# Optimization experiments

Measured on AMD Instinct MI355X. Metric: run time of the kernel, lower is better.

Reference implementation:

```python
import jax, jax.numpy as jnp
import numpy as np

EMB_DIM, D_H, BSZ, SEQ = 2048, 128, 4, 4096
HALF = D_H // 2


def apply_rope(x, sin, cos):
    # x: [b, s, d]; sin/cos: [s, d//2]; interleaved-pair rotation
    b, s, d = x.shape
    xr = x.reshape(b, s, d // 2, 2)
    x0, x1 = xr[..., 0], xr[..., 1]
    r0 = x0 * cos - x1 * sin
    r1 = x1 * cos + x0 * sin
    return jnp.stack([r0, r1], axis=-1).reshape(b, s, d)


def setup_inputs() -> dict:
    key = jax.random.key(0)
    kx, kq, kk, kv = jax.random.split(key, 4)
    x = jax.random.normal(kx, (BSZ, SEQ, EMB_DIM), dtype=jnp.float32)
    # causal mask (1 = attend, 0 = masked), matching mask[q,:] slicing in source
    mask = jnp.tril(jnp.ones((SEQ, SEQ), dtype=jnp.int32))
    # standard RoPE angle tables: [seq, d_h//2]
    inv_freq = 1.0 / (10000.0 ** (jnp.arange(HALF, dtype=jnp.float32) / HALF))
    angles = jnp.arange(SEQ, dtype=jnp.float32)[:, None] * inv_freq[None, :]
    sin, cos = jnp.sin(angles), jnp.cos(angles)
    scale = 1.0 / np.sqrt(EMB_DIM)
    W_Q = jax.random.normal(kq, (EMB_DIM, D_H), dtype=jnp.float32) * scale
    W_K = jax.random.normal(kk, (EMB_DIM, D_H), dtype=jnp.float32) * scale
    W_V = jax.random.normal(kv, (EMB_DIM, D_H), dtype=jnp.float32) * scale
    return {"x": x, "mask": mask, "sin": sin, "cos": cos,
            "W_Q": W_Q, "W_K": W_K, "W_V": W_V}


def reference(x, mask, sin, cos, W_Q, W_V, W_K):
    # QKV projections
    Q = apply_rope(x @ W_Q, sin, cos)  # [b, s, d_h]
    K = apply_rope(x @ W_K, sin, cos)  # [b, s, d_h]
    V = x @ W_V                        # [b, s, d_h]
    # The source's chunked loop is exactly full masked attention over all K/V.
    scores = jnp.einsum('bqd,bkd->bqk', Q, K) / jnp.sqrt(jnp.float32(D_H))
    scores = jnp.where(mask[None, :, :] == 0, -jnp.inf, scores)
    attn = jax.nn.softmax(scores, axis=-1)
    return jnp.einsum('bqk,bkd->bqd', attn, V)
```

## Files before the change

kernel.cpp:

```cpp
#include <hip/hip_runtime.h>
#include <stdint.h>
#include <stddef.h>

typedef __bf16 bf16;
typedef __bf16 bf16x8 __attribute__((ext_vector_type(8)));
typedef float f32x4 __attribute__((ext_vector_type(4)));
typedef unsigned int uint32x2 __attribute__((ext_vector_type(2)));
typedef unsigned int uint32x4 __attribute__((ext_vector_type(4)));

typedef const __attribute__((address_space(1))) uint32_t GU32;
typedef __attribute__((address_space(3))) uint32_t LU32;

__device__ __forceinline__ f32x4 mfma16(bf16x8 a, bf16x8 b, f32x4 c) {
  return __builtin_amdgcn_mfma_f32_16x16x32_bf16(a, b, c, 0, 0, 0);
}
__device__ __forceinline__ void gload16(const void* g, void* l) {
  __builtin_amdgcn_global_load_lds((GU32*)g, (LU32*)l, 16, 0, 0);
}

__global__ __launch_bounds__(256) void k_prep(const float* __restrict__ Wq,
                                              const float* __restrict__ Wk,
                                              const float* __restrict__ Wv,
                                              bf16* __restrict__ Wct) {
  __shared__ float tile[64][65];
  const int tid = threadIdx.x;
  const int widx = blockIdx.x >> 6, rem = blockIdx.x & 63;
  const int k0 = (rem >> 1) * 64, n0 = (rem & 1) * 64;
  const float* W = (widx == 0) ? Wq : (widx == 1) ? Wk : Wv;
  const int rg = tid >> 4, cq = tid & 15;
#pragma unroll
  for (int i = 0; i < 4; ++i) {
    int krow = i * 16 + rg;
    f32x4 v = *(const f32x4*)(W + (size_t)(k0 + krow) * 128 + n0 + cq * 4);
#pragma unroll
    for (int j = 0; j < 4; ++j) tile[krow][cq * 4 + j] = v[j];
  }
  __syncthreads();
#pragma unroll
  for (int i = 0; i < 4; ++i) {
    int nrow = i * 16 + rg;
    union { bf16 h[4]; uint32x2 u; } pk;
#pragma unroll
    for (int j = 0; j < 4; ++j) pk.h[j] = (bf16)tile[cq * 4 + j][nrow];
    *(uint32x2*)(Wct + (size_t)(widx * 128 + n0 + nrow) * 2048 + k0 + cq * 4) = pk.u;
  }
}

__global__ __launch_bounds__(256, 2) void k_proj(
    const float* __restrict__ x, const float* __restrict__ sint, const float* __restrict__ cost,
    const bf16* __restrict__ Wct, bf16* __restrict__ Qg, bf16* __restrict__ Kg,
    bf16* __restrict__ Vtg) {
  __shared__ __align__(16) uint8_t smem[65536];
  const int tid = threadIdx.x;
  const int lane = tid & 63, w = tid >> 6;
  const int l15 = lane & 15, l16 = lane >> 4;
  const int logical = (blockIdx.x & 7) * 64 + (blockIdx.x >> 3);
  const int nb = logical & 1, mb = logical >> 1;
  const int wm = w >> 1, wn = w & 1;
  const int arow = tid >> 2, aj = tid & 3;

  f32x4 acc[2][6] = {};
  f32x4 areg[4];

  const float* abase = x + (size_t)(mb * 64 + arow) * 2048 + aj * 16;

  auto stageB = [&](int buf, int ks) {
    uint8_t* bbm = smem + buf * 32768 + 8192;
    int k0 = ks * 64;
#pragma unroll
    for (int i = 0; i < 6; ++i) {
      int L = i * 4096 + tid * 16;
      int n = L >> 7, cp = (L >> 4) & 7;
      int cc = cp ^ (n & 7);
      const uint8_t* src = (const uint8_t*)Wct + (((size_t)(nb * 192 + n) * 2048 + k0 + cc * 8) << 1);
      gload16(src, bbm + i * 4096 + w * 1024);
    }
  };
  auto loadA = [&](int ks) {
    const f32x4* p = (const f32x4*)(abase + ks * 64);
#pragma unroll
    for (int i = 0; i < 4; ++i) areg[i] = p[i];
  };
  auto writeA = [&](int buf) {
    uint8_t* ab = smem + buf * 32768;
#pragma unroll
    for (int h = 0; h < 2; ++h) {
      union { bf16 v[8]; uint32x4 u; } pk;
#pragma unroll
      for (int e = 0; e < 8; ++e) pk.v[e] = (bf16)areg[h * 2 + (e >> 2)][e & 3];
      int c = aj * 2 + h;
      *(uint32x4*)(ab + arow * 128 + (((c ^ (arow & 7)) & 7) << 4)) = pk.u;
    }
  };
  auto compute = [&](int buf) {
    uint8_t* ab = smem + buf * 32768;
    uint8_t* bbm = ab + 8192;
#pragma unroll
    for (int kk = 0; kk < 2; ++kk) {
      bf16x8 af[2], bv[6];
#pragma unroll
      for (int mt = 0; mt < 2; ++mt) {
        int ml = wm * 32 + mt * 16 + l15;
        af[mt] = *(const bf16x8*)(ab + ml * 128 + (((kk * 4 + l16) ^ (ml & 7)) << 4));
      }
#pragma unroll
      for (int nt = 0; nt < 6; ++nt) {
        int nl = wn * 96 + nt * 16 + l15;
        bv[nt] = *(const bf16x8*)(bbm + nl * 128 + (((kk * 4 + l16) ^ (nl & 7)) << 4));
      }
#pragma unroll
      for (int mt = 0; mt < 2; ++mt)
#pragma unroll
        for (int nt = 0; nt < 6; ++nt)
          acc[mt][nt] = mfma16(af[mt], bv[nt], acc[mt][nt]);
    }
  };

  stageB(0, 0);
  loadA(0);
  writeA(0);
  __syncthreads();
  for (int ks = 0; ks < 32; ++ks) {
    int cur = ks & 1;
    if (ks + 1 < 32) { stageB(cur ^ 1, ks + 1); loadA(ks + 1); }
    compute(cur);
    if (ks + 1 < 32) writeA(cur ^ 1);
    __syncthreads();
  }

#pragma unroll
  for (int mt = 0; mt < 2; ++mt) {
    int gm = mb * 64 + wm * 32 + mt * 16 + l16 * 4;
    int bb = gm >> 12, s0 = gm & 4095;
#pragma unroll
    for (int nt = 0; nt < 6; ++nt) {
      int jcol = nb * 192 + wn * 96 + nt * 16 + l15;
      f32x4 v = acc[mt][nt];
      if (jcol < 256) {
        int p = (jcol & 127) >> 1;
        bool even = ((jcol & 1) == 0);
#pragma unroll
        for (int r = 0; r < 4; ++r) {
          float pv = __shfl_xor(v[r], 1);
          int s = s0 + r;
          float cs = cost[s * 64 + p], sn = sint[s * 64 + p];
          float nv = even ? (v[r] * cs - pv * sn) : (v[r] * cs + pv * sn);
          bf16 hb = (bf16)nv;
          if (jcol < 128) Qg[((size_t)(bb << 12) + s) * 128 + jcol] = hb;
          else            Kg[((size_t)(bb << 12) + s) * 128 + jcol - 128] = hb;
        }
      } else {
        int d = jcol - 256;
        union { bf16 h[4]; uint32x2 u; } pk;
#pragma unroll
        for (int r = 0; r < 4; ++r) pk.h[r] = (bf16)v[r];
        *(uint32x2*)((uint8_t*)Vtg + (((size_t)(bb << 7) + d) * 4096 + s0) * 2) = pk.u;
      }
    }
  }
}

__global__ __launch_bounds__(256, 2) void k_attn(
    const bf16* __restrict__ Qg, const bf16* __restrict__ Kg, const bf16* __restrict__ Vtg,
    float* __restrict__ PO, float* __restrict__ ML) {
  __shared__ __align__(16) uint8_t smem[81920];
  const int tid = threadIdx.x;
  const int lane = tid & 63, w = tid >> 6;
  const int l15 = lane & 15, l16 = lane >> 4;

  int gid = blockIdx.x;
  int b = gid / 80, rr = gid % 80;
  int j, c;
  if (rr < 8)       { j = rr;                 c = 0; }
  else if (rr < 24) { j = 8 + ((rr - 8) >> 1);  c = (rr - 8) & 1; }
  else if (rr < 48) { j = 16 + (rr - 24) / 3;   c = (rr - 24) % 3; }
  else              { j = 24 + ((rr - 48) >> 2); c = (rr - 48) & 3; }

  const int q0w = j * 128 + w * 32;
  const int kv_lo = c * 1024;
  const int kv_hi = min((c + 1) * 1024, (j + 1) * 128);
  const int T = (kv_hi - kv_lo) >> 6;

  bf16x8 qf[2][4];
#pragma unroll
  for (int qt = 0; qt < 2; ++qt)
#pragma unroll
    for (int kk = 0; kk < 4; ++kk)
      qf[qt][kk] = *(const bf16x8*)(Qg + ((size_t)(b << 12) + q0w + qt * 16 + l15) * 128 + kk * 32 + l16 * 8);

  f32x4 o[2][8] = {};
  float m_r[2] = {-1e30f, -1e30f};
  float l_r[2] = {0.f, 0.f};
  uint8_t* pb = smem + 65536 + w * 4096;

  auto stage = [&](int t) {
    uint8_t* kb = smem + (t & 1) * 32768;
    uint8_t* vb = kb + 16384;
    int kv0 = kv_lo + t * 64;
#pragma unroll
    for (int i = 0; i < 4; ++i) {
      int L = i * 4096 + tid * 16;
      {
        int kv = L >> 8, cp = (L >> 4) & 15, cc = cp ^ (kv & 7);
        const uint8_t* src = (const uint8_t*)Kg + ((size_t)((b << 12) + kv0 + kv) << 8) + (cc << 4);
        gload16(src, kb + i * 4096 + w * 1024);
      }
      {
        int d = L >> 7, cp = (L >> 4) & 7, cc = cp ^ (d & 7);
        const uint8_t* src = (const uint8_t*)Vtg + ((size_t)(((b << 7) + d) << 12) + kv0 + (cc << 3)) * 2;
        gload16(src, vb + i * 4096 + w * 1024);
      }
    }
  };

  stage(0);
  __syncthreads();

  for (int t = 0; t < T; ++t) {
    if (t + 1 < T) stage(t + 1);
    const int kv0 = kv_lo + t * 64;
    if (kv0 <= q0w + 31) {
      uint8_t* kb = smem + (t & 1) * 32768;
      uint8_t* vb = kb + 16384;
      f32x4 sfr[4][2] = {};
#pragma unroll
      for (int kk = 0; kk < 4; ++kk) {
#pragma unroll
        for (int kvt = 0; kvt < 4; ++kvt) {
          int kvl = kvt * 16 + l15;
          bf16x8 kf = *(const bf16x8*)(kb + (kvl << 8) + (((kk * 4 + l16) ^ (kvl & 7)) << 4));
#pragma unroll
          for (int qt = 0; qt < 2; ++qt)
            sfr[kvt][qt] = mfma16(kf, qf[qt][kk], sfr[kvt][qt]);
        }
      }
      const bool need_mask = (kv0 + 63 > q0w);
      const float scale = 0.08838834764831845f;
#pragma unroll
      for (int qt = 0; qt < 2; ++qt) {
        const int q = q0w + qt * 16 + l15;
        float pvv[4][4];
        float tmax = -1e30f;
#pragma unroll
        for (int kvt = 0; kvt < 4; ++kvt)
#pragma unroll
          for (int r = 0; r < 4; ++r) {
            float sv = sfr[kvt][qt][r] * scale;
            if (need_mask) {
              int kv = kv0 + kvt * 16 + l16 * 4 + r;
              if (kv > q) sv = -1e30f;
            }
            pvv[kvt][r] = sv;
            tmax = fmaxf(tmax, sv);
          }
        tmax = fmaxf(tmax, __shfl_xor(tmax, 16));
        tmax = fmaxf(tmax, __shfl_xor(tmax, 32));
        float mnew = fmaxf(m_r[qt], tmax);
        float corr = __expf(m_r[qt] - mnew);
        m_r[qt] = mnew;
        float rs = 0.f;
#pragma unroll
        for (int kvt = 0; kvt < 4; ++kvt)
#pragma unroll
          for (int r = 0; r < 4; ++r) {
            float p = __expf(pvv[kvt][r] - mnew);
            pvv[kvt][r] = p;
            rs += p;
          }
        rs += __shfl_xor(rs, 16);
        rs += __shfl_xor(rs, 32);
        l_r[qt] = l_r[qt] * corr + rs;
        const int qrow = qt * 16 + l15;
#pragma unroll
        for (int kvt = 0; kvt < 4; ++kvt) {
          union { bf16 h[4]; uint32x2 u; } pk;
#pragma unroll
          for (int r = 0; r < 4; ++r) pk.h[r] = (bf16)pvv[kvt][r];
          int kv2 = kvt * 32 + l16 * 8;
          *(uint32x2*)(pb + qrow * 128 + ((((kv2 >> 4) ^ (qrow & 7)) << 4) | (kv2 & 15))) = pk.u;
        }
#pragma unroll
        for (int r = 0; r < 4; ++r) {
          float cr = __shfl(corr, l16 * 4 + r);
#pragma unroll
          for (int dt = 0; dt < 8; ++dt) o[qt][dt][r] *= cr;
        }
      }
#pragma unroll
      for (int kvb = 0; kvb < 2; ++kvb) {
        bf16x8 pa[2];
#pragma unroll
        for (int qt = 0; qt < 2; ++qt) {
          int qrow = qt * 16 + l15;
          int kv2 = kvb * 64 + l16 * 16;
          pa[qt] = *(const bf16x8*)(pb + qrow * 128 + (((kv2 >> 4) ^ (qrow & 7)) << 4));
        }
#pragma unroll
        for (int dt = 0; dt < 8; ++dt) {
          int d = dt * 16 + l15;
          bf16x8 vf = *(const bf16x8*)(vb + (d << 7) + (((kvb * 4 + l16) ^ (d & 7)) << 4));
#pragma unroll
          for (int qt = 0; qt < 2; ++qt)
            o[qt][dt] = mfma16(pa[qt], vf, o[qt][dt]);
        }
      }
    }
    __syncthreads();
  }

  float* POb = PO + (size_t)((b * 32 + j) * 4 + c) * 16384;
#pragma unroll
  for (int qt = 0; qt < 2; ++qt)
#pragma unroll
    for (int dt = 0; dt < 8; ++dt)
#pragma unroll
      for (int r = 0; r < 4; ++r)
        POb[(w * 32 + qt * 16 + l16 * 4 + r) * 128 + dt * 16 + l15] = o[qt][dt][r];
  float* MLb = ML + (size_t)((b * 32 + j) * 4 + c) * 256;
  if (l16 == 0) {
#pragma unroll
    for (int qt = 0; qt < 2; ++qt) {
      MLb[w * 32 + qt * 16 + l15] = m_r[qt];
      MLb[128 + w * 32 + qt * 16 + l15] = l_r[qt];
    }
  }
}

__global__ void k_combine(const float* __restrict__ PO, const float* __restrict__ ML,
                          float* __restrict__ out) {
  int blk = blockIdx.x;
  int b = blk >> 5, j = blk & 31;
  int nc = 1 + (j >> 3);
  int t = threadIdx.x;
  int q = t >> 1, half = t & 1;
  const float* MLb = ML + (size_t)(b * 32 + j) * 4 * 256;
  float mv[4], lv[4];
  float ms = -1e30f;
  for (int cc = 0; cc < nc; ++cc) {
    mv[cc] = MLb[cc * 256 + q];
    lv[cc] = MLb[cc * 256 + 128 + q];
    ms = fmaxf(ms, mv[cc]);
  }
  float wgt[4];
  float den = 0.f;
  for (int cc = 0; cc < nc; ++cc) { wgt[cc] = __expf(mv[cc] - ms); den += wgt[cc] * lv[cc]; }
  float inv = 1.f / den;
  const float* POb = PO + (size_t)(b * 32 + j) * 4 * 16384 + q * 128 + half * 64;
  float* ob = out + ((size_t)(b << 12) + j * 128 + q) * 128 + half * 64;
  for (int d = 0; d < 64; d += 4) {
    f32x4 a = {0.f, 0.f, 0.f, 0.f};
    for (int cc = 0; cc < nc; ++cc) {
      f32x4 v = *(const f32x4*)(POb + cc * 16384 + d);
      a += v * wgt[cc];
    }
    a *= inv;
    *(f32x4*)(ob + d) = a;
  }
}

extern "C" void kernel_launch(void* const* d_in, const int* in_sizes, int n_in,
                              void* d_out, int out_size, void* d_ws, size_t ws_size,
                              hipStream_t stream) {
  const float* x = (const float*)d_in[0];
  const float* sint = (const float*)d_in[2];
  const float* cost = (const float*)d_in[3];
  const float* Wq = (const float*)d_in[4];
  const float* Wk = (const float*)d_in[5];
  const float* Wv = (const float*)d_in[6];
  uint8_t* ws = (uint8_t*)d_ws;

  bf16* Wct = (bf16*)(ws + 0x0);
  bf16* Qg  = (bf16*)(ws + 0x180000);
  bf16* Kg  = (bf16*)(ws + 0x580000);
  bf16* Vtg = (bf16*)(ws + 0x980000);
  float* PO = (float*)(ws + 0xD80000);
  float* ML = (float*)(ws + 0x2D80000);
  float* out = (float*)d_out;

  hipLaunchKernelGGL(k_prep, dim3(192), dim3(256), 0, stream, Wq, Wk, Wv, Wct);
  hipLaunchKernelGGL(k_proj, dim3(512), dim3(256), 0, stream, x, sint, cost, Wct, Qg, Kg, Vtg);
  hipLaunchKernelGGL(k_attn, dim3(320), dim3(256), 0, stream, Qg, Kg, Vtg, PO, ML);
  hipLaunchKernelGGL(k_combine, dim3(128), dim3(256), 0, stream, PO, ML, out);
}
```

Baseline: 140.7 us.

## Deepen projection GEMM pipeline with double register A buffers and manual waitcnts

Rewrites the k_proj main loop to prefetch x tiles two steps ahead into alternating register buffers. The loop is unrolled by two, and the full __syncthreads is replaced with explicit vmcnt/lgkmcnt waits plus s_barrier, so the newest A loads stay in flight across the barrier. The compute step now loads all LDS fragments for both k-substeps before issuing the MFMAs, and raises wave priority with s_setprio around the MFMA block. The aim is to hide global load latency in the projection GEMM, at the cost of more registers and reliance on hand-counted vmcnt values matching the compiler's load order.

```diff
diff --git a/kernel.cpp b/kernel.cpp
--- a/kernel.cpp
+++ b/kernel.cpp
@@ -60,7 +60,7 @@
   const int arow = tid >> 2, aj = tid & 3;
 
   f32x4 acc[2][6] = {};
-  f32x4 areg[4];
+  f32x4 regA[4], regB[4];
 
   const float* abase = x + (size_t)(mb * 64 + arow) * 2048 + aj * 16;
 
@@ -76,18 +76,18 @@
       gload16(src, bbm + i * 4096 + w * 1024);
     }
   };
-  auto loadA = [&](int ks) {
+  auto loadA = [&](int ks, f32x4* r) {
     const f32x4* p = (const f32x4*)(abase + ks * 64);
 #pragma unroll
-    for (int i = 0; i < 4; ++i) areg[i] = p[i];
+    for (int i = 0; i < 4; ++i) r[i] = p[i];
   };
-  auto writeA = [&](int buf) {
+  auto writeA = [&](int buf, const f32x4* r) {
     uint8_t* ab = smem + buf * 32768;
 #pragma unroll
     for (int h = 0; h < 2; ++h) {
       union { bf16 v[8]; uint32x4 u; } pk;
 #pragma unroll
-      for (int e = 0; e < 8; ++e) pk.v[e] = (bf16)areg[h * 2 + (e >> 2)][e & 3];
+      for (int e = 0; e < 8; ++e) pk.v[e] = (bf16)r[h * 2 + (e >> 2)][e & 3];
       int c = aj * 2 + h;
       *(uint32x4*)(ab + arow * 128 + (((c ^ (arow & 7)) & 7) << 4)) = pk.u;
     }
@@ -95,38 +95,68 @@
   auto compute = [&](int buf) {
     uint8_t* ab = smem + buf * 32768;
     uint8_t* bbm = ab + 8192;
+    bf16x8 af[2][2], bv[2][6];
 #pragma unroll
     for (int kk = 0; kk < 2; ++kk) {
-      bf16x8 af[2], bv[6];
 #pragma unroll
       for (int mt = 0; mt < 2; ++mt) {
         int ml = wm * 32 + mt * 16 + l15;
-        af[mt] = *(const bf16x8*)(ab + ml * 128 + (((kk * 4 + l16) ^ (ml & 7)) << 4));
+        af[kk][mt] = *(const bf16x8*)(ab + ml * 128 + (((kk * 4 + l16) ^ (ml & 7)) << 4));
       }
 #pragma unroll
       for (int nt = 0; nt < 6; ++nt) {
         int nl = wn * 96 + nt * 16 + l15;
-        bv[nt] = *(const bf16x8*)(bbm + nl * 128 + (((kk * 4 + l16) ^ (nl & 7)) << 4));
-      }
+        bv[kk][nt] = *(const bf16x8*)(bbm + nl * 128 + (((kk * 4 + l16) ^ (nl & 7)) << 4));
+      }
+    }
+    __builtin_amdgcn_s_setprio(1);
+#pragma unroll
+    for (int kk = 0; kk < 2; ++kk)
 #pragma unroll
       for (int mt = 0; mt < 2; ++mt)
 #pragma unroll
         for (int nt = 0; nt < 6; ++nt)
-          acc[mt][nt] = mfma16(af[mt], bv[nt], acc[mt][nt]);
-    }
+          acc[mt][nt] = mfma16(af[kk][mt], bv[kk][nt], acc[mt][nt]);
+    __builtin_amdgcn_s_setprio(0);
   };
 
+  loadA(0, regA);
   stageB(0, 0);
-  loadA(0);
-  writeA(0);
-  __syncthreads();
-  for (int ks = 0; ks < 32; ++ks) {
-    int cur = ks & 1;
-    if (ks + 1 < 32) { stageB(cur ^ 1, ks + 1); loadA(ks + 1); }
-    compute(cur);
-    if (ks + 1 < 32) writeA(cur ^ 1);
-    __syncthreads();
-  }
+  loadA(1, regB);
+  writeA(0, regA);
+  asm volatile("s_waitcnt vmcnt(4)" ::: "memory");
+  asm volatile("s_waitcnt lgkmcnt(0)" ::: "memory");
+  __builtin_amdgcn_s_barrier();
+
+  for (int ks = 0; ks < 30; ks += 2) {
+    {
+      stageB(1, ks + 1);
+      loadA(ks + 2, regA);
+      compute(0);
+      writeA(1, regB);
+      asm volatile("s_waitcnt vmcnt(4)" ::: "memory");
+      asm volatile("s_waitcnt lgkmcnt(0)" ::: "memory");
+      __builtin_amdgcn_s_barrier();
+    }
+    {
+      stageB(0, ks + 2);
+      loadA(ks + 3, regB);
+      compute(1);
+      writeA(0, regA);
+      asm volatile("s_waitcnt vmcnt(4)" ::: "memory");
+      asm volatile("s_waitcnt lgkmcnt(0)" ::: "memory");
+      __builtin_amdgcn_s_barrier();
+    }
+  }
+  {
+    stageB(1, 31);
+    compute(0);
+    writeA(1, regB);
+    asm volatile("s_waitcnt vmcnt(0)" ::: "memory");
+    asm volatile("s_waitcnt lgkmcnt(0)" ::: "memory");
+    __builtin_amdgcn_s_barrier();
+  }
+  compute(1);
 
 #pragma unroll
   for (int mt = 0; mt < 2; ++mt) {
```

Result: faster. 132.2 us (-6.0%).

## Pre-swizzle weights into MFMA fragment order and enlarge projection tiles to 128 rows

Applied to the files above, without the earlier changes.

The prep kernel now writes the bf16 weights directly in per-k-step MFMA fragment order, so the projection kernel can stage B with contiguous global-to-LDS loads and read fragments without XOR swizzling. The projection kernel moves to 512-thread blocks covering 128 rows with an 8-wave 2x4 layout, and raises wave priority around the MFMA section. The aims are to cut address arithmetic, get more A reuse per B tile and lower the block count, in exchange for more LDS per block (80 KB) and a launch bound that restricts registers.

```diff
diff --git a/kernel.cpp b/kernel.cpp
--- a/kernel.cpp
+++ b/kernel.cpp
@@ -21,7 +21,7 @@
 __global__ __launch_bounds__(256) void k_prep(const float* __restrict__ Wq,
                                               const float* __restrict__ Wk,
                                               const float* __restrict__ Wv,
-                                              bf16* __restrict__ Wct) {
+                                              bf16* __restrict__ WB) {
   __shared__ float tile[64][65];
   const int tid = threadIdx.x;
   const int widx = blockIdx.x >> 6, rem = blockIdx.x & 63;
@@ -37,82 +37,85 @@
   }
   __syncthreads();
 #pragma unroll
-  for (int i = 0; i < 4; ++i) {
-    int nrow = i * 16 + rg;
-    union { bf16 h[4]; uint32x2 u; } pk;
-#pragma unroll
-    for (int j = 0; j < 4; ++j) pk.h[j] = (bf16)tile[cq * 4 + j][nrow];
-    *(uint32x2*)(Wct + (size_t)(widx * 128 + n0 + nrow) * 2048 + k0 + cq * 4) = pk.u;
-  }
-}
-
-__global__ __launch_bounds__(256, 2) void k_proj(
+  for (int gi = 0; gi < 2; ++gi) {
+    int G = tid * 2 + gi;
+    int n_local = G >> 3, kg = G & 7;
+    union { bf16 h[8]; uint32x4 u; } pk;
+#pragma unroll
+    for (int j = 0; j < 8; ++j) pk.h[j] = (bf16)tile[kg * 8 + j][n_local];
+    int n_glob = widx * 128 + n0 + n_local;
+    int k_glob = k0 + kg * 8;
+    int nb = n_glob / 192, nr = n_glob % 192;
+    int ngl = nr >> 4, l15g = nr & 15;
+    int ks = k_glob >> 6, kk = (k_glob >> 5) & 1, l16g = (k_glob >> 3) & 3;
+    size_t gaddr = ((size_t)(nb * 32 + ks) * 1536) + ((ngl * 2 + kk) * 64 + l16g * 16 + l15g);
+    *(uint32x4*)((uint8_t*)WB + gaddr * 16) = pk.u;
+  }
+}
+
+__global__ __launch_bounds__(512, 4) void k_proj(
     const float* __restrict__ x, const float* __restrict__ sint, const float* __restrict__ cost,
-    const bf16* __restrict__ Wct, bf16* __restrict__ Qg, bf16* __restrict__ Kg,
+    const bf16* __restrict__ WB, bf16* __restrict__ Qg, bf16* __restrict__ Kg,
     bf16* __restrict__ Vtg) {
-  __shared__ __align__(16) uint8_t smem[65536];
+  __shared__ __align__(16) uint8_t smem[81920];
   const int tid = threadIdx.x;
   const int lane = tid & 63, w = tid >> 6;
   const int l15 = lane & 15, l16 = lane >> 4;
-  const int logical = (blockIdx.x & 7) * 64 + (blockIdx.x >> 3);
+  const int logical = (blockIdx.x & 7) * 32 + (blockIdx.x >> 3);
   const int nb = logical & 1, mb = logical >> 1;
-  const int wm = w >> 1, wn = w & 1;
+  const int wm = w >> 2, wn = w & 3;
   const int arow = tid >> 2, aj = tid & 3;
 
-  f32x4 acc[2][6] = {};
-  f32x4 areg[4];
-
-  const float* abase = x + (size_t)(mb * 64 + arow) * 2048 + aj * 16;
+  f32x4 acc[4][3] = {};
+  f32x4 ar[4];
+
+  const float* abase = x + (size_t)(mb * 128 + arow) * 2048 + aj * 16;
+  const uint8_t* wbase = (const uint8_t*)WB + (size_t)nb * 32 * 24576;
 
   auto stageB = [&](int buf, int ks) {
-    uint8_t* bbm = smem + buf * 32768 + 8192;
-    int k0 = ks * 64;
-#pragma unroll
-    for (int i = 0; i < 6; ++i) {
-      int L = i * 4096 + tid * 16;
-      int n = L >> 7, cp = (L >> 4) & 7;
-      int cc = cp ^ (n & 7);
-      const uint8_t* src = (const uint8_t*)Wct + (((size_t)(nb * 192 + n) * 2048 + k0 + cc * 8) << 1);
-      gload16(src, bbm + i * 4096 + w * 1024);
-    }
+    uint8_t* bbm = smem + 32768 + buf * 24576;
+    const uint8_t* src = wbase + (size_t)ks * 24576 + tid * 16;
+#pragma unroll
+    for (int i = 0; i < 3; ++i)
+      gload16(src + i * 8192, bbm + i * 8192 + tid * 16);
   };
   auto loadA = [&](int ks) {
     const f32x4* p = (const f32x4*)(abase + ks * 64);
 #pragma unroll
-    for (int i = 0; i < 4; ++i) areg[i] = p[i];
+    for (int i = 0; i < 4; ++i) ar[i] = p[i];
   };
   auto writeA = [&](int buf) {
-    uint8_t* ab = smem + buf * 32768;
+    uint8_t* ab = smem + buf * 16384;
 #pragma unroll
     for (int h = 0; h < 2; ++h) {
       union { bf16 v[8]; uint32x4 u; } pk;
 #pragma unroll
-      for (int e = 0; e < 8; ++e) pk.v[e] = (bf16)areg[h * 2 + (e >> 2)][e & 3];
+      for (int e = 0; e < 8; ++e) pk.v[e] = (bf16)ar[h * 2 + (e >> 2)][e & 3];
       int c = aj * 2 + h;
       *(uint32x4*)(ab + arow * 128 + (((c ^ (arow & 7)) & 7) << 4)) = pk.u;
     }
   };
   auto compute = [&](int buf) {
-    uint8_t* ab = smem + buf * 32768;
-    uint8_t* bbm = ab + 8192;
+    uint8_t* ab = smem + buf * 16384;
+    uint8_t* bbm = smem + 32768 + buf * 24576;
 #pragma unroll
     for (int kk = 0; kk < 2; ++kk) {
-      bf16x8 af[2], bv[6];
-#pragma unroll
-      for (int mt = 0; mt < 2; ++mt) {
-        int ml = wm * 32 + mt * 16 + l15;
-        af[mt] = *(const bf16x8*)(ab + ml * 128 + (((kk * 4 + l16) ^ (ml & 7)) << 4));
-      }
-#pragma unroll
-      for (int nt = 0; nt < 6; ++nt) {
-        int nl = wn * 96 + nt * 16 + l15;
-        bv[nt] = *(const bf16x8*)(bbm + nl * 128 + (((kk * 4 + l16) ^ (nl & 7)) << 4));
-      }
-#pragma unroll
-      for (int mt = 0; mt < 2; ++mt)
-#pragma unroll
-        for (int nt = 0; nt < 6; ++nt)
+      bf16x8 af[4], bv[3];
+#pragma unroll
+      for (int mt = 0; mt < 4; ++mt) {
+        int row = wm * 64 + mt * 16 + l15;
+        af[mt] = *(const bf16x8*)(ab + row * 128 + (((kk * 4 + l16) ^ (l15 & 7)) << 4));
+      }
+#pragma unroll
+      for (int nt = 0; nt < 3; ++nt)
+        bv[nt] = *(const bf16x8*)(bbm + ((((wn * 3 + nt) * 2 + kk) * 64 + lane) << 4));
+      __builtin_amdgcn_s_setprio(1);
+#pragma unroll
+      for (int mt = 0; mt < 4; ++mt)
+#pragma unroll
+        for (int nt = 0; nt < 3; ++nt)
           acc[mt][nt] = mfma16(af[mt], bv[nt], acc[mt][nt]);
+      __builtin_amdgcn_s_setprio(0);
     }
   };
 
@@ -129,12 +132,12 @@
   }
 
 #pragma unroll
-  for (int mt = 0; mt < 2; ++mt) {
-    int gm = mb * 64 + wm * 32 + mt * 16 + l16 * 4;
+  for (int mt = 0; mt < 4; ++mt) {
+    int gm = mb * 128 + wm * 64 + mt * 16 + l16 * 4;
     int bb = gm >> 12, s0 = gm & 4095;
 #pragma unroll
-    for (int nt = 0; nt < 6; ++nt) {
-      int jcol = nb * 192 + wn * 96 + nt * 16 + l15;
+    for (int nt = 0; nt < 3; ++nt) {
+      int jcol = nb * 192 + wn * 48 + nt * 16 + l15;
       f32x4 v = acc[mt][nt];
       if (jcol < 256) {
         int p = (jcol & 127) >> 1;
@@ -369,7 +372,7 @@
   const float* Wv = (const float*)d_in[6];
   uint8_t* ws = (uint8_t*)d_ws;
 
-  bf16* Wct = (bf16*)(ws + 0x0);
+  bf16* WB  = (bf16*)(ws + 0x0);
   bf16* Qg  = (bf16*)(ws + 0x180000);
   bf16* Kg  = (bf16*)(ws + 0x580000);
   bf16* Vtg = (bf16*)(ws + 0x980000);
@@ -377,8 +380,8 @@
   float* ML = (float*)(ws + 0x2D80000);
   float* out = (float*)d_out;
 
-  hipLaunchKernelGGL(k_prep, dim3(192), dim3(256), 0, stream, Wq, Wk, Wv, Wct);
-  hipLaunchKernelGGL(k_proj, dim3(512), dim3(256), 0, stream, x, sint, cost, Wct, Qg, Kg, Vtg);
+  hipLaunchKernelGGL(k_prep, dim3(192), dim3(256), 0, stream, Wq, Wk, Wv, WB);
+  hipLaunchKernelGGL(k_proj, dim3(256), dim3(512), 0, stream, x, sint, cost, WB, Qg, Kg, Vtg);
   hipLaunchKernelGGL(k_attn, dim3(320), dim3(256), 0, stream, Qg, Kg, Vtg, PO, ML);
   hipLaunchKernelGGL(k_combine, dim3(128), dim3(256), 0, stream, PO, ML, out);
 }
```

After: 133.0 us. -5.5%, faster.
